# Kernel tuning notes

Measured on AMD Instinct MI355X. Metric: run time of the kernel, lower is better.

The kernel has to match this reference:

```python
import jax, jax.numpy as jnp
import numpy as np

H = 512  # hidden_dimension
B = 32
S = 2048


def setup_inputs() -> dict:
    key = jax.random.key(0)
    k1, k2, k3, k4, k5, k6 = jax.random.split(key, 6)
    decoder_hide = jax.random.normal(k1, (B, H), dtype=jnp.float32)
    encoder_out = jax.random.normal(k2, (B, S, 2 * H), dtype=jnp.float32)
    mask = jax.random.randint(k3, (B, S), 0, 2, dtype=jnp.int32)
    bound = 1.0 / np.sqrt(3 * H)
    W_attn = jax.random.uniform(k4, (3 * H, H), minval=-bound, maxval=bound, dtype=jnp.float32)
    b_attn = jax.random.uniform(k5, (H,), minval=-bound, maxval=bound, dtype=jnp.float32)
    bound_v = 1.0 / np.sqrt(H)
    v_w = jax.random.uniform(k6, (H,), minval=-bound_v, maxval=bound_v, dtype=jnp.float32)
    return {"decoder_hide": decoder_hide, "encoder_out": encoder_out, "mask": mask,
            "W_attn": W_attn, "b_attn": b_attn, "v_w": v_w}


def reference(decoder_hide, encoder_out, mask, W_attn, b_attn, v_w):
    # Split the concat-linear: cat((h, enc)) @ W == h @ W[:H] + enc @ W[H:]
    W_h = W_attn[:H]        # [H, H]
    W_e = W_attn[H:]        # [2H, H]
    dec_proj = decoder_hide @ W_h + b_attn                 # [B, H]
    enc_proj = jnp.einsum('bse,eh->bsh', encoder_out, W_e)  # [B, S, H]
    energy = jnp.tanh(enc_proj + dec_proj[:, None, :])      # [B, S, H]
    attention = jnp.einsum('bsh,h->bs', energy, v_w)        # [B, S]
    attention = jnp.where(mask == 0, jnp.float32(-100000.0), attention)
    return jax.nn.softmax(attention, axis=1)
```

## Files before the change

### kernel.cpp

```cpp
#include <hip/hip_runtime.h>
#include <hip/hip_bf16.h>
#include <math.h>

#define Hdim 512
#define Bdim 32
#define Sdim 2048
#define Kdim 1024
#define Mtot (Bdim * Sdim)

#define BM 64
#define BK 64

typedef __attribute__((ext_vector_type(8))) short short8;
typedef __attribute__((ext_vector_type(4))) float floatx4;

__device__ __forceinline__ short f2bf(float f) {
    union { float f; unsigned u; } v; v.f = f;
    unsigned r = v.u + 0x7fffu + ((v.u >> 16) & 1u);
    return (short)(r >> 16);
}

__device__ __forceinline__ short8 cvt8(float4 a, float4 b) {
    union { short8 s; __hip_bfloat162 h[4]; } u;
    u.h[0] = __float22bfloat162_rn(make_float2(a.x, a.y));
    u.h[1] = __float22bfloat162_rn(make_float2(a.z, a.w));
    u.h[2] = __float22bfloat162_rn(make_float2(b.x, b.y));
    u.h[3] = __float22bfloat162_rn(make_float2(b.z, b.w));
    return u.s;
}

__device__ __forceinline__ float fast_tanh(float x) {
    float ax = fabsf(x);
    float e  = __expf(-2.0f * ax);
    float r  = (1.0f - e) * __builtin_amdgcn_rcpf(1.0f + e);
    return copysignf(r, x);
}

__global__ __launch_bounds__(256) void prep_kernel(
    const float* __restrict__ W_attn, const float* __restrict__ dec,
    const float* __restrict__ b_attn, short* __restrict__ Wbp,
    float* __restrict__ dec_proj)
{
    const int t = threadIdx.x;
    if (blockIdx.x < 512) {
        const float* We = W_attn + Hdim * Hdim;
        __shared__ short tile[32][33];
        const int k0 = (blockIdx.x >> 4) * 32;
        const int n0 = (blockIdx.x & 15) * 32;
        const int r = t >> 5, c = t & 31;
        #pragma unroll
        for (int rr = 0; rr < 4; ++rr)
            tile[r + rr * 8][c] = f2bf(We[(size_t)(k0 + r + rr * 8) * Hdim + n0 + c]);
        __syncthreads();
        if (t < 128) {
            const int n_loc = t >> 2;
            const int q     = t & 3;
            const int nt    = (n0 + n_loc) >> 4;
            const int lnn   = (n0 + n_loc) & 15;
            const int ks    = k0 >> 5;
            short8 v;
            #pragma unroll
            for (int r2 = 0; r2 < 8; ++r2) v[r2] = tile[q * 8 + r2][n_loc];
            ((short8*)Wbp)[((nt * 32 + ks) * 64) + q * 16 + lnn] = v;
        }
    } else {
        __shared__ float partl[2][128];
        const int bid = blockIdx.x - 512;
        const int b  = bid >> 2;
        const int cb = bid & 3;
        const int c  = cb * 128 + (t & 127);
        const int kh = t >> 7;
        float acc = 0.0f;
        const int kbeg = kh * 256, kend = kbeg + 256;
        #pragma unroll 8
        for (int k = kbeg; k < kend; ++k)
            acc = fmaf(dec[b * Hdim + k], W_attn[(size_t)k * Hdim + c], acc);
        partl[kh][t & 127] = acc;
        __syncthreads();
        if (t < 128)
            dec_proj[b * Hdim + cb * 128 + t] = partl[0][t] + partl[1][t] + b_attn[cb * 128 + t];
    }
}

__global__ __launch_bounds__(512, 4) void scores_kernel(
    const float* __restrict__ enc,
    const short* __restrict__ Wbp,
    const float* __restrict__ dec_proj,
    const float* __restrict__ v_w,
    float* __restrict__ scores)
{
    __shared__ __align__(16) short Asm[2 * BM * BK];
    __shared__ float redl[BM][8];

    const int t    = threadIdx.x;
    const int row0 = blockIdx.x * BM;
    const int b    = row0 / Sdim;

    const int w    = t >> 6;
    const int lane = t & 63;
    const int ln   = lane & 15;
    const int quad = lane >> 4;

    const int sm = t >> 3;
    const int sq = t & 7;
    const float* Ag = enc + (size_t)(row0 + sm) * Kdim + sq * 8;
    const int awo = sm * BK + ((sq ^ (sm & 7)) * 8);

    int arow[4];
    #pragma unroll
    for (int i = 0; i < 4; ++i) arow[i] = (i * 16 + ln) * BK;
    const int pf0 = (quad       ^ (ln & 7)) * 8;
    const int pf1 = ((4 + quad) ^ (ln & 7)) * 8;

    const short8* Bp = ((const short8*)Wbp) + lane;

    floatx4 acc[4][4];
    #pragma unroll
    for (int i = 0; i < 4; ++i)
        #pragma unroll
        for (int j = 0; j < 4; ++j)
            acc[i][j] = (floatx4)(0.0f);

    float4 ra0, ra1;
    {
        const float4* g = (const float4*)Ag;
        ra0 = g[0]; ra1 = g[1];
    }

    for (int kt = 0; kt < Kdim; kt += BK) {
        short* Ab = Asm + ((kt >> 6) & 1) * (BM * BK);
        *(short8*)&Ab[awo] = cvt8(ra0, ra1);
        __syncthreads();

        const int ks = kt >> 5;
        short8 b0[4], b1[4];
        #pragma unroll
        for (int j = 0; j < 4; ++j)
            b0[j] = Bp[(size_t)((w * 4 + j) * 32 + ks) * 64];
        #pragma unroll
        for (int j = 0; j < 4; ++j)
            b1[j] = Bp[(size_t)((w * 4 + j) * 32 + ks + 1) * 64];

        if (kt + BK < Kdim) {
            const float4* g = (const float4*)(Ag + kt + BK);
            ra0 = g[0]; ra1 = g[1];
        }

        short8 af[4];
        #pragma unroll
        for (int i = 0; i < 4; ++i) af[i] = *(const short8*)&Ab[arow[i] + pf0];
        #pragma unroll
        for (int i = 0; i < 4; ++i)
            #pragma unroll
            for (int j = 0; j < 4; ++j)
                acc[i][j] = __builtin_amdgcn_mfma_f32_16x16x32_bf16(
                                af[i], b0[j], acc[i][j], 0, 0, 0);
        #pragma unroll
        for (int i = 0; i < 4; ++i) af[i] = *(const short8*)&Ab[arow[i] + pf1];
        #pragma unroll
        for (int i = 0; i < 4; ++i)
            #pragma unroll
            for (int j = 0; j < 4; ++j)
                acc[i][j] = __builtin_amdgcn_mfma_f32_16x16x32_bf16(
                                af[i], b1[j], acc[i][j], 0, 0, 0);
    }

    float dpv[4], vwv[4];
    #pragma unroll
    for (int j = 0; j < 4; ++j) {
        int col = w * 64 + j * 16 + ln;
        dpv[j] = dec_proj[b * Hdim + col];
        vwv[j] = v_w[col];
    }
    #pragma unroll
    for (int i = 0; i < 4; ++i) {
        #pragma unroll
        for (int reg = 0; reg < 4; ++reg) {
            float s = 0.0f;
            #pragma unroll
            for (int j = 0; j < 4; ++j) {
                float x = acc[i][j][reg] + dpv[j];
                s = fmaf(vwv[j], fast_tanh(x), s);
            }
            s += __shfl_xor(s, 1, 64);
            s += __shfl_xor(s, 2, 64);
            s += __shfl_xor(s, 4, 64);
            s += __shfl_xor(s, 8, 64);
            if (ln == 0)
                redl[i * 16 + quad * 4 + reg][w] = s;
        }
    }
    __syncthreads();
    if (t < BM) {
        float s = 0.0f;
        #pragma unroll
        for (int wv = 0; wv < 8; ++wv) s += redl[t][wv];
        scores[row0 + t] = s;
    }
}

__global__ __launch_bounds__(256) void softmax_kernel(
    const float* __restrict__ scores, const int* __restrict__ mask,
    float* __restrict__ out)
{
    __shared__ float sred[8];
    const int b = blockIdx.x;
    const int t = threadIdx.x;
    const int lane = t & 63;
    const int wid  = t >> 6;

    float x[8];
    float m = -1e30f;
    #pragma unroll
    for (int j = 0; j < 8; ++j) {
        int idx = b * Sdim + j * 256 + t;
        float v = scores[idx];
        if (mask[idx] == 0) v = -100000.0f;
        x[j] = v;
        m = fmaxf(m, v);
    }
    #pragma unroll
    for (int off = 32; off >= 1; off >>= 1)
        m = fmaxf(m, __shfl_xor(m, off, 64));
    if (lane == 0) sred[wid] = m;
    __syncthreads();
    m = fmaxf(fmaxf(sred[0], sred[1]), fmaxf(sred[2], sred[3]));

    float s = 0.0f;
    #pragma unroll
    for (int j = 0; j < 8; ++j) {
        float e = __expf(x[j] - m);
        x[j] = e;
        s += e;
    }
    #pragma unroll
    for (int off = 32; off >= 1; off >>= 1)
        s += __shfl_xor(s, off, 64);
    if (lane == 0) sred[4 + wid] = s;
    __syncthreads();
    s = sred[4] + sred[5] + sred[6] + sred[7];

    const float inv = 1.0f / s;
    #pragma unroll
    for (int j = 0; j < 8; ++j)
        out[b * Sdim + j * 256 + t] = x[j] * inv;
}

extern "C" void kernel_launch(void* const* d_in, const int* in_sizes, int n_in,
                              void* d_out, int out_size, void* d_ws, size_t ws_size,
                              hipStream_t stream) {
    const float* dec  = (const float*)d_in[0];
    const float* enc  = (const float*)d_in[1];
    const int*   mask = (const int*)  d_in[2];
    const float* W    = (const float*)d_in[3];
    const float* ba   = (const float*)d_in[4];
    const float* vw   = (const float*)d_in[5];
    float* out = (float*)d_out;

    float* dec_proj = (float*)d_ws;
    short* Wbp      = (short*)(dec_proj + Bdim * Hdim);
    float* scores   = (float*)(Wbp + Hdim * Kdim);

    prep_kernel<<<640, 256, 0, stream>>>(W, dec, ba, Wbp, dec_proj);
    scores_kernel<<<Mtot / BM, 512, 0, stream>>>(enc, Wbp, dec_proj, vw, scores);
    softmax_kernel<<<Bdim, 256, 0, stream>>>(scores, mask, out);
}
```

Baseline: 426.7 us.

## Double block rows to 128 with 16 waves and two-deep global prefetch

Result: slower. 445.4 us (+4.4%).

```diff
diff --git a/kernel.cpp b/kernel.cpp
--- a/kernel.cpp
+++ b/kernel.cpp
@@ -8,7 +8,7 @@
 #define Kdim 1024
 #define Mtot (Bdim * Sdim)
 
-#define BM 64
+#define BM 128
 #define BK 64
 
 typedef __attribute__((ext_vector_type(8))) short short8;
@@ -82,7 +82,69 @@
     }
 }
 
-__global__ __launch_bounds__(512, 4) void scores_kernel(
+__device__ __forceinline__ void kstep(
+    int kt, short* __restrict__ Ab, float4& ra, float4& rb,
+    const float* __restrict__ Ag, const short8* __restrict__ Bp,
+    int w, int abase, int pf0, int pf1, int awo,
+    floatx4 (&acc)[8][2])
+{
+    const size_t ks = (size_t)(kt >> 5);
+    const size_t nt0 = (size_t)(w * 2 + 0) * 32;
+    const size_t nt1 = (size_t)(w * 2 + 1) * 32;
+    short8 b0[2], b1[2];
+    b0[0] = Bp[(nt0 + ks) * 64];
+    b0[1] = Bp[(nt1 + ks) * 64];
+    b1[0] = Bp[(nt0 + ks + 1) * 64];
+    b1[1] = Bp[(nt1 + ks + 1) * 64];
+
+    *(short8*)&Ab[awo] = cvt8(ra, rb);
+    __syncthreads();
+
+    if (kt + 2 * BK < Kdim) {
+        const float4* g = (const float4*)(Ag + kt + 2 * BK);
+        ra = g[0]; rb = g[1];
+    }
+
+    short8 af[4];
+    #pragma unroll
+    for (int i2 = 0; i2 < 4; ++i2)
+        af[i2] = *(const short8*)&Ab[abase + i2 * 1024 + pf0];
+    #pragma unroll
+    for (int i2 = 0; i2 < 4; ++i2)
+        #pragma unroll
+        for (int j = 0; j < 2; ++j)
+            acc[i2][j] = __builtin_amdgcn_mfma_f32_16x16x32_bf16(
+                             af[i2], b0[j], acc[i2][j], 0, 0, 0);
+    #pragma unroll
+    for (int i2 = 0; i2 < 4; ++i2)
+        af[i2] = *(const short8*)&Ab[abase + (i2 + 4) * 1024 + pf0];
+    #pragma unroll
+    for (int i2 = 0; i2 < 4; ++i2)
+        #pragma unroll
+        for (int j = 0; j < 2; ++j)
+            acc[i2 + 4][j] = __builtin_amdgcn_mfma_f32_16x16x32_bf16(
+                                 af[i2], b0[j], acc[i2 + 4][j], 0, 0, 0);
+    #pragma unroll
+    for (int i2 = 0; i2 < 4; ++i2)
+        af[i2] = *(const short8*)&Ab[abase + i2 * 1024 + pf1];
+    #pragma unroll
+    for (int i2 = 0; i2 < 4; ++i2)
+        #pragma unroll
+        for (int j = 0; j < 2; ++j)
+            acc[i2][j] = __builtin_amdgcn_mfma_f32_16x16x32_bf16(
+                             af[i2], b1[j], acc[i2][j], 0, 0, 0);
+    #pragma unroll
+    for (int i2 = 0; i2 < 4; ++i2)
+        af[i2] = *(const short8*)&Ab[abase + (i2 + 4) * 1024 + pf1];
+    #pragma unroll
+    for (int i2 = 0; i2 < 4; ++i2)
+        #pragma unroll
+        for (int j = 0; j < 2; ++j)
+            acc[i2 + 4][j] = __builtin_amdgcn_mfma_f32_16x16x32_bf16(
+                                 af[i2], b1[j], acc[i2 + 4][j], 0, 0, 0);
+}
+
+__global__ __launch_bounds__(1024, 4) void scores_kernel(
     const float* __restrict__ enc,
     const short* __restrict__ Wbp,
     const float* __restrict__ dec_proj,
@@ -90,7 +152,7 @@
     float* __restrict__ scores)
 {
     __shared__ __align__(16) short Asm[2 * BM * BK];
-    __shared__ float redl[BM][8];
+    __shared__ float redl[BM][16];
 
     const int t    = threadIdx.x;
     const int row0 = blockIdx.x * BM;
@@ -106,79 +168,42 @@
     const float* Ag = enc + (size_t)(row0 + sm) * Kdim + sq * 8;
     const int awo = sm * BK + ((sq ^ (sm & 7)) * 8);
 
-    int arow[4];
-    #pragma unroll
-    for (int i = 0; i < 4; ++i) arow[i] = (i * 16 + ln) * BK;
-    const int pf0 = (quad       ^ (ln & 7)) * 8;
-    const int pf1 = ((4 + quad) ^ (ln & 7)) * 8;
+    const int abase = ln * BK;
+    const int pf0 = (quad ^ (ln & 7)) * 8;
+    const int pf1 = pf0 ^ 32;
 
     const short8* Bp = ((const short8*)Wbp) + lane;
 
-    floatx4 acc[4][4];
-    #pragma unroll
-    for (int i = 0; i < 4; ++i)
-        #pragma unroll
-        for (int j = 0; j < 4; ++j)
+    floatx4 acc[8][2];
+    #pragma unroll
+    for (int i = 0; i < 8; ++i)
+        #pragma unroll
+        for (int j = 0; j < 2; ++j)
             acc[i][j] = (floatx4)(0.0f);
 
-    float4 ra0, ra1;
-    {
-        const float4* g = (const float4*)Ag;
-        ra0 = g[0]; ra1 = g[1];
-    }
-
-    for (int kt = 0; kt < Kdim; kt += BK) {
-        short* Ab = Asm + ((kt >> 6) & 1) * (BM * BK);
-        *(short8*)&Ab[awo] = cvt8(ra0, ra1);
-        __syncthreads();
-
-        const int ks = kt >> 5;
-        short8 b0[4], b1[4];
-        #pragma unroll
-        for (int j = 0; j < 4; ++j)
-            b0[j] = Bp[(size_t)((w * 4 + j) * 32 + ks) * 64];
-        #pragma unroll
-        for (int j = 0; j < 4; ++j)
-            b1[j] = Bp[(size_t)((w * 4 + j) * 32 + ks + 1) * 64];
-
-        if (kt + BK < Kdim) {
-            const float4* g = (const float4*)(Ag + kt + BK);
-            ra0 = g[0]; ra1 = g[1];
-        }
-
-        short8 af[4];
-        #pragma unroll
-        for (int i = 0; i < 4; ++i) af[i] = *(const short8*)&Ab[arow[i] + pf0];
-        #pragma unroll
-        for (int i = 0; i < 4; ++i)
-            #pragma unroll
-            for (int j = 0; j < 4; ++j)
-                acc[i][j] = __builtin_amdgcn_mfma_f32_16x16x32_bf16(
-                                af[i], b0[j], acc[i][j], 0, 0, 0);
-        #pragma unroll
-        for (int i = 0; i < 4; ++i) af[i] = *(const short8*)&Ab[arow[i] + pf1];
-        #pragma unroll
-        for (int i = 0; i < 4; ++i)
-            #pragma unroll
-            for (int j = 0; j < 4; ++j)
-                acc[i][j] = __builtin_amdgcn_mfma_f32_16x16x32_bf16(
-                                af[i], b1[j], acc[i][j], 0, 0, 0);
-    }
-
-    float dpv[4], vwv[4];
-    #pragma unroll
-    for (int j = 0; j < 4; ++j) {
-        int col = w * 64 + j * 16 + ln;
+    float4 r0a, r0b, r1a, r1b;
+    { const float4* g = (const float4*)Ag;        r0a = g[0]; r0b = g[1]; }
+    { const float4* g = (const float4*)(Ag + BK); r1a = g[0]; r1b = g[1]; }
+
+    for (int kt = 0; kt < Kdim; kt += 2 * BK) {
+        kstep(kt,      Asm,           r0a, r0b, Ag, Bp, w, abase, pf0, pf1, awo, acc);
+        kstep(kt + BK, Asm + BM * BK, r1a, r1b, Ag, Bp, w, abase, pf0, pf1, awo, acc);
+    }
+
+    float dpv[2], vwv[2];
+    #pragma unroll
+    for (int j = 0; j < 2; ++j) {
+        const int col = w * 32 + j * 16 + ln;
         dpv[j] = dec_proj[b * Hdim + col];
         vwv[j] = v_w[col];
     }
     #pragma unroll
-    for (int i = 0; i < 4; ++i) {
+    for (int i = 0; i < 8; ++i) {
         #pragma unroll
         for (int reg = 0; reg < 4; ++reg) {
             float s = 0.0f;
             #pragma unroll
-            for (int j = 0; j < 4; ++j) {
+            for (int j = 0; j < 2; ++j) {
                 float x = acc[i][j][reg] + dpv[j];
                 s = fmaf(vwv[j], fast_tanh(x), s);
             }
@@ -194,7 +219,7 @@
     if (t < BM) {
         float s = 0.0f;
         #pragma unroll
-        for (int wv = 0; wv < 8; ++wv) s += redl[t][wv];
+        for (int wv = 0; wv < 16; ++wv) s += redl[t][wv];
         scores[row0 + t] = s;
     }
 }
@@ -262,6 +287,6 @@
     float* scores   = (float*)(Wbp + Hdim * Kdim);
 
     prep_kernel<<<640, 256, 0, stream>>>(W, dec, ba, Wbp, dec_proj);
-    scores_kernel<<<Mtot / BM, 512, 0, stream>>>(enc, Wbp, dec_proj, vw, scores);
+    scores_kernel<<<Mtot / BM, 1024, 0, stream>>>(enc, Wbp, dec_proj, vw, scores);
     softmax_kernel<<<Bdim, 256, 0, stream>>>(scores, mask, out);
 }
```
